# Optimization experiments

Hardware: AMD Instinct MI355X
Metric: run time of the kernel (lower is better)

The kernel has to match this reference:

```python
import jax, jax.numpy as jnp
import numpy as np

B, S, D = 8, 4096, 256
NUM_WINDOW = 8
WIN = S // NUM_WINDOW          # 512
H = 2                          # num_heads
K = D                          # key_dim = d_model per source
DFF = 1024
LN_EPS = 1e-3                  # keras LayerNormalization default epsilon


def _layer_norm(x, g, b):
    mu = jnp.mean(x, axis=-1, keepdims=True)
    var = jnp.mean(jnp.square(x - mu), axis=-1, keepdims=True)
    return (x - mu) * jax.lax.rsqrt(var + LN_EPS) * g + b


def setup_inputs() -> dict:
    key = jax.random.key(0)
    ks = jax.random.split(key, 12)
    s = 0.02
    inp = {
        "x": jax.random.normal(ks[0], (B, S, D), dtype=jnp.float32),
        # MHA projections (keras MultiHeadAttention layout)
        "Wq": jax.random.normal(ks[1], (D, H, K), dtype=jnp.float32) * s,
        "bq": jnp.zeros((H, K), dtype=jnp.float32),
        "Wk": jax.random.normal(ks[2], (D, H, K), dtype=jnp.float32) * s,
        "bk": jnp.zeros((H, K), dtype=jnp.float32),
        "Wv": jax.random.normal(ks[3], (D, H, K), dtype=jnp.float32) * s,
        "bv": jnp.zeros((H, K), dtype=jnp.float32),
        "Wo": jax.random.normal(ks[4], (H, K, D), dtype=jnp.float32) * s,
        "bo": jnp.zeros((D,), dtype=jnp.float32),
        "ln1_g": jnp.ones((D,), dtype=jnp.float32),
        "ln1_b": jnp.zeros((D,), dtype=jnp.float32),
        # FeedForward
        "W1": jax.random.normal(ks[5], (D, DFF), dtype=jnp.float32) * s,
        "b1": jnp.zeros((DFF,), dtype=jnp.float32),
        "W2": jax.random.normal(ks[6], (DFF, D), dtype=jnp.float32) * s,
        "b2": jnp.zeros((D,), dtype=jnp.float32),
        "ln2_g": jnp.ones((D,), dtype=jnp.float32),
        "ln2_b": jnp.zeros((D,), dtype=jnp.float32),
    }
    return inp


def reference(x, Wq, bq, Wk, bk, Wv, bv, Wo, bo, ln1_g, ln1_b,
              W1, b1, W2, b2, ln2_g, ln2_b):
    # --- Localized self-attention: block-diagonal over NUM_WINDOW windows ---
    xw = x.reshape(B, NUM_WINDOW, WIN, D)               # [b, w, s, d]
    q = jnp.einsum('bwsd,dhk->bwshk', xw, Wq) + bq      # [b, w, s, h, k]
    k = jnp.einsum('bwsd,dhk->bwshk', xw, Wk) + bk
    v = jnp.einsum('bwsd,dhk->bwshk', xw, Wv) + bv
    scores = jnp.einsum('bwshk,bwthk->bwhst', q, k) / jnp.sqrt(
        jnp.asarray(K, dtype=x.dtype))                  # [b, w, h, s, t]
    attn = jax.nn.softmax(scores, axis=-1)
    ctx = jnp.einsum('bwhst,bwthk->bwshk', attn, v)     # [b, w, s, h, k]
    attn_out = jnp.einsum('bwshk,hkd->bwsd', ctx, Wo) + bo
    attn_out = attn_out.reshape(B, S, D)                # concat over windows
    x = _layer_norm(x + attn_out, ln1_g, ln1_b)
    # --- FeedForward (dropout inactive at inference) ---
    h = jax.nn.relu(x @ W1 + b1)
    ff = h @ W2 + b2
    return _layer_norm(x + ff, ln2_g, ln2_b)
```

## Files before the change

kernel.cpp:

```cpp
#include <hip/hip_runtime.h>

typedef unsigned short u16;
typedef short short8 __attribute__((ext_vector_type(8)));
typedef float f32x4 __attribute__((ext_vector_type(4)));

#define AS1C const __attribute__((address_space(1))) void*
#define AS3P __attribute__((address_space(3))) void*
#define VMW(n) asm volatile("s_waitcnt vmcnt(" #n ")" ::: "memory")
#define SCHEDB() __builtin_amdgcn_sched_barrier(0)

__device__ __forceinline__ u16 f2b(float f) {
  unsigned u = __float_as_uint(f);
  return (u16)((u + 0x7fffu + ((u >> 16) & 1u)) >> 16);
}
__device__ __forceinline__ float b2f(u16 h) {
  return __uint_as_float((unsigned)h << 16);
}

#define BB 8
#define SS 4096
#define DD 256
#define MTOK (BB*SS)

#define OFF_WQKVT  ((size_t)0)
#define OFF_WOT    ((size_t)786432)
#define OFF_W1T    ((size_t)1048576)
#define OFF_W2T    ((size_t)1572864)
#define OFF_BQKV   ((size_t)2097152)
#define OFF_XB     ((size_t)2103296)
#define OFF_QKV    ((size_t)18880512)
#define OFF_YB     ((size_t)52434944)
#define OFF_HB     ((size_t)69212160)
#define OFF_VT     ((size_t)119543808)
#define OFF_CTX    ((size_t)153098240)

__global__ __launch_bounds__(256) void cast_x_kernel(const float* __restrict__ x,
                                                     u16* __restrict__ xb) {
  size_t i = ((size_t)blockIdx.x * 256 + threadIdx.x) * 4;
  float4 v = *(const float4*)(x + i);
  ushort4 o;
  o.x = f2b(v.x); o.y = f2b(v.y); o.z = f2b(v.z); o.w = f2b(v.w);
  *(ushort4*)(xb + i) = o;
}

__global__ __launch_bounds__(256) void prep_w_kernel(
    const float* __restrict__ Wq, const float* __restrict__ Wk, const float* __restrict__ Wv,
    const float* __restrict__ Wo, const float* __restrict__ W1, const float* __restrict__ W2,
    const float* __restrict__ bq, const float* __restrict__ bk, const float* __restrict__ bv,
    u16* __restrict__ wqkvt, u16* __restrict__ wot, u16* __restrict__ w1t,
    u16* __restrict__ w2t, float* __restrict__ bqkv)
{
  for (int i = blockIdx.x * 256 + threadIdx.x; i < 1050112; i += 1024 * 256) {
    if (i < 393216) {
      int n = i >> 8, d = i & 255;
      const float* W = (n < 512) ? Wq : (n < 1024) ? Wk : Wv;
      int nn = n & 511;
      wqkvt[i] = f2b(W[d * 512 + nn]);
    } else if (i < 524288) {
      int j = i - 393216;
      int dout = j >> 9, hk = j & 511;
      wot[j] = f2b(Wo[hk * 256 + dout]);
    } else if (i < 786432) {
      int j = i - 524288;
      int f = j >> 8, d = j & 255;
      w1t[j] = f2b(W1[d * 1024 + f]);
    } else if (i < 1048576) {
      int j = i - 786432;
      int d = j >> 10, f = j & 1023;
      w2t[j] = f2b(W2[f * 256 + d]);
    } else {
      int n = i - 1048576;
      bqkv[n] = (n < 512) ? bq[n] : (n < 1024) ? bk[n - 512] : bv[n - 1024];
    }
  }
}

__global__ __launch_bounds__(256) void gemm_nres(
    const u16* __restrict__ A, const u16* __restrict__ BT,
    const float* __restrict__ bias, u16* __restrict__ C,
    u16* __restrict__ vt, int N, int vbase, int relu)
{
  __shared__ __align__(16) u16 lds[24576];
  const int tid = threadIdx.x, lane = tid & 63, wid = tid >> 6;
  const int ln = lane & 15, quad = lane >> 4;
  const int pn = blockIdx.x >> 5;
  const int mg = blockIdx.x & 31;
  const int wno = (wid >> 1) << 5;
  const int wmo = (wid & 1) << 4;
  const long mbase = (long)mg << 10;
  const int nb = pn << 6;
  const u16* Bp = BT + (size_t)nb * 256;
  const u16* Ap = A + (size_t)mbase * 256;

#pragma unroll
  for (int p = 0; p < 8; p++) {
    const int s = p * 256 + tid;
    const int row = s >> 5, pc = s & 31;
    const int c = pc ^ (row & 31);
    __builtin_amdgcn_global_load_lds(
        (AS1C)(Bp + (size_t)row * 256 + c * 8), (AS3P)(lds + s * 8), 16, 0, 0);
  }
  __syncthreads();
  short8 breg[2][8];
#pragma unroll
  for (int j = 0; j < 2; j++) {
    const int row = wno + j * 16 + ln;
#pragma unroll
    for (int ks = 0; ks < 8; ks++)
      breg[j][ks] = *(const short8*)(lds + row * 256 + (((ks << 2) + quad) ^ (row & 31)) * 8);
  }
  const float4 b40 = *(const float4*)(bias + nb + wno + quad * 4);
  const float4 b41 = *(const float4*)(bias + nb + wno + 16 + quad * 4);
  __syncthreads();

#pragma unroll
  for (int sl = 0; sl < 2; sl++) {
    const u16* As = Ap + (size_t)sl * 32 * 256;
#pragma unroll
    for (int p = 0; p < 4; p++) {
      const int s = p * 256 + tid;
      const int row = s >> 5, pc = s & 31;
      const int c = pc ^ (row & 31);
      __builtin_amdgcn_global_load_lds(
          (AS1C)(As + (size_t)row * 256 + c * 8), (AS3P)(lds + sl * 8192 + s * 8), 16, 0, 0);
    }
  }

  for (int it = 0; it < 32; it++) {
    if (it == 0)            VMW(4);
    else if (it == 31)      VMW(0);
    else if (nb < vbase)    VMW(6);
    else                    VMW(12);
    SCHEDB();
    __builtin_amdgcn_s_barrier();
    SCHEDB();
    const u16* Ab = lds + (it % 3) * 8192;
    f32x4 acc[2];
    acc[0] = (f32x4){0.f, 0.f, 0.f, 0.f};
    acc[1] = (f32x4){0.f, 0.f, 0.f, 0.f};
    const int r0 = wmo + ln;
#pragma unroll
    for (int ks = 0; ks < 8; ks++) {
      const short8 a0 = *(const short8*)(Ab + r0 * 256 + (((ks << 2) + quad) ^ (r0 & 31)) * 8);
      acc[0] = __builtin_amdgcn_mfma_f32_16x16x32_bf16(breg[0][ks], a0, acc[0], 0, 0, 0);
      acc[1] = __builtin_amdgcn_mfma_f32_16x16x32_bf16(breg[1][ks], a0, acc[1], 0, 0, 0);
    }
    const long m = mbase + it * 32 + wmo + ln;
    if (nb < vbase) {
#pragma unroll
      for (int j = 0; j < 2; j++) {
        const int n0 = nb + wno + j * 16 + quad * 4;
        f32x4 v = acc[j];
        const float4 b4 = j ? b41 : b40;
        v[0] += b4.x; v[1] += b4.y; v[2] += b4.z; v[3] += b4.w;
        if (relu) {
#pragma unroll
          for (int r = 0; r < 4; r++) v[r] = fmaxf(v[r], 0.f);
        }
        ushort4 ob;
        ob.x = f2b(v[0]); ob.y = f2b(v[1]); ob.z = f2b(v[2]); ob.w = f2b(v[3]);
        *(ushort4*)(C + (size_t)m * N + n0) = ob;
      }
    } else {
      const int bw = (int)(m >> 9), t = (int)(m & 511);
#pragma unroll
      for (int j = 0; j < 2; j++) {
        const int n0 = nb + wno + j * 16 + quad * 4;
        const int rel = n0 - vbase;
        const int h = rel >> 8, k0 = rel & 255;
        u16* vp = vt + (size_t)(bw * 2 + h) * 131072 + (size_t)k0 * 512 + t;
        const float4 b4 = j ? b41 : b40;
        vp[0]    = f2b(acc[j][0] + b4.x);
        vp[512]  = f2b(acc[j][1] + b4.y);
        vp[1024] = f2b(acc[j][2] + b4.z);
        vp[1536] = f2b(acc[j][3] + b4.w);
      }
    }
    if (it < 30) {
      const u16* An = Ap + (size_t)(it + 2) * 32 * 256;
      u16* Ax = lds + ((it + 2) % 3) * 8192;
#pragma unroll
      for (int p = 0; p < 4; p++) {
        const int s = p * 256 + tid;
        const int row = s >> 5, pc = s & 31;
        const int c = pc ^ (row & 31);
        __builtin_amdgcn_global_load_lds(
            (AS1C)(An + (size_t)row * 256 + c * 8), (AS3P)(Ax + s * 8), 16, 0, 0);
      }
    }
  }
}

__global__ __launch_bounds__(512, 4) void attn_fused(const u16* __restrict__ qkv,
                                                     const u16* __restrict__ vt,
                                                     u16* __restrict__ ctx)
{
  __shared__ __align__(16) u16 lds[38912];
  const int tid = threadIdx.x, lane = tid & 63, wid = tid >> 6;
  const int ln = lane & 15, quad = lane >> 4;
  const int bat = blockIdx.x & 127, mt = blockIdx.x >> 7;
  const int bw = bat >> 1, h = bat & 1;
  const u16* Qb = qkv + (size_t)bw * 786432 + (size_t)h * 256 + (size_t)(mt * 64) * 1536;
  const u16* Kb = qkv + (size_t)bw * 786432 + 512 + (size_t)h * 256;
  const u16* Vb = vt + (size_t)bat * 131072;
  const int wn = wid * 64;
  const int qsw = (ln >> 1) & 3;
  float* red1 = (float*)(lds + 36864);
  float* red2 = red1 + 512;

  f32x4 acc[4][4];
#pragma unroll
  for (int i = 0; i < 4; i++)
#pragma unroll
    for (int j = 0; j < 4; j++) acc[i][j] = (f32x4){0.f, 0.f, 0.f, 0.f};

  if (tid < 256) {
    const int row = tid >> 2;
    const int c = (tid & 3) ^ ((row >> 1) & 3);
    __builtin_amdgcn_global_load_lds(
        (AS1C)(Qb + (size_t)row * 1536 + c * 8), (AS3P)(lds + tid * 8), 16, 0, 0);
  }
#pragma unroll
  for (int p = 0; p < 4; p++) {
    const int s = p * 512 + tid;
    const int row = s >> 2;
    const int c = (s & 3) ^ ((row >> 1) & 3);
    __builtin_amdgcn_global_load_lds(
        (AS1C)(Kb + (size_t)row * 1536 + c * 8), (AS3P)(lds + 4096 + s * 8), 16, 0, 0);
  }

  for (int ki = 0; ki < 8; ki++) {
    const int cur = ki & 1;
    __syncthreads();
    if (ki < 7) {
      const int kt = (ki + 1) * 32, nxt = cur ^ 1;
      if (tid < 256) {
        const int row = tid >> 2;
        const int c = (tid & 3) ^ ((row >> 1) & 3);
        __builtin_amdgcn_global_load_lds(
            (AS1C)(Qb + (size_t)row * 1536 + kt + c * 8),
            (AS3P)(lds + nxt * 2048 + tid * 8), 16, 0, 0);
      }
#pragma unroll
      for (int p = 0; p < 4; p++) {
        const int s = p * 512 + tid;
        const int row = s >> 2;
        const int c = (s & 3) ^ ((row >> 1) & 3);
        __builtin_amdgcn_global_load_lds(
            (AS1C)(Kb + (size_t)row * 1536 + kt + c * 8),
            (AS3P)(lds + 4096 + nxt * 16384 + s * 8), 16, 0, 0);
      }
    }
    short8 a[4], b[4];
#pragma unroll
    for (int i = 0; i < 4; i++)
      a[i] = *(const short8*)(lds + cur * 2048 + ((i * 16 + ln) * 4 + (quad ^ qsw)) * 8);
#pragma unroll
    for (int j = 0; j < 4; j++)
      b[j] = *(const short8*)(lds + 4096 + cur * 16384 + ((wn + j * 16 + ln) * 4 + (quad ^ qsw)) * 8);
    __builtin_amdgcn_s_setprio(1);
#pragma unroll
    for (int i = 0; i < 4; i++)
#pragma unroll
      for (int j = 0; j < 4; j++)
        acc[i][j] = __builtin_amdgcn_mfma_f32_16x16x32_bf16(b[j], a[i], acc[i][j], 0, 0, 0);
    __builtin_amdgcn_s_setprio(0);
  }

  float rowmax[4], rowsum[4];
#pragma unroll
  for (int i = 0; i < 4; i++) {
    float m = -1e30f;
#pragma unroll
    for (int j = 0; j < 4; j++)
#pragma unroll
      for (int r = 0; r < 4; r++) m = fmaxf(m, acc[i][j][r]);
    m = fmaxf(m, __shfl_xor(m, 16));
    m = fmaxf(m, __shfl_xor(m, 32));
    if (quad == 0) red1[wid * 64 + i * 16 + ln] = m;
  }
  __syncthreads();

#pragma unroll
  for (int p = 0; p < 4; p++) {
    const int s = p * 512 + tid;
    const int row = s >> 3, pc = s & 7;
    const int cc = pc ^ (row & 7);
    __builtin_amdgcn_global_load_lds(
        (AS1C)(Vb + (size_t)row * 512 + cc * 8), (AS3P)(lds + s * 8), 16, 0, 0);
  }

#pragma unroll
  for (int i = 0; i < 4; i++) {
    float m = -1e30f;
#pragma unroll
    for (int w = 0; w < 8; w++) m = fmaxf(m, red1[w * 64 + i * 16 + ln]);
    rowmax[i] = m;
  }
#pragma unroll
  for (int i = 0; i < 4; i++) {
    float s = 0.f;
#pragma unroll
    for (int j = 0; j < 4; j++)
#pragma unroll
      for (int r = 0; r < 4; r++) {
        const float e = __expf((acc[i][j][r] - rowmax[i]) * 0.0625f);
        acc[i][j][r] = e; s += e;
      }
    s += __shfl_xor(s, 16);
    s += __shfl_xor(s, 32);
    if (quad == 0) red2[wid * 64 + i * 16 + ln] = s;
  }
  __syncthreads();
#pragma unroll
  for (int i = 0; i < 4; i++) {
    float s = 0.f;
#pragma unroll
    for (int w = 0; w < 8; w++) s += red2[w * 64 + i * 16 + ln];
    rowsum[i] = 1.f / s;
  }

  ushort4 pb[4][4];
#pragma unroll
  for (int i = 0; i < 4; i++)
#pragma unroll
    for (int j = 0; j < 4; j++) {
      pb[i][j].x = f2b(acc[i][j][0] * rowsum[i]);
      pb[i][j].y = f2b(acc[i][j][1] * rowsum[i]);
      pb[i][j].z = f2b(acc[i][j][2] * rowsum[i]);
      pb[i][j].w = f2b(acc[i][j][3] * rowsum[i]);
    }

  u16* Pb = lds + 32768;
  const int wno = wid * 32;
  f32x4 o[4][2];
#pragma unroll
  for (int i = 0; i < 4; i++) {
    o[i][0] = (f32x4){0.f, 0.f, 0.f, 0.f};
    o[i][1] = (f32x4){0.f, 0.f, 0.f, 0.f};
  }

  for (int c = 0; c < 8; c++) {
    __syncthreads();
    if (wid == c) {
#pragma unroll
      for (int i = 0; i < 4; i++)
#pragma unroll
        for (int j = 0; j < 4; j++)
          *(ushort4*)(Pb + (i * 16 + ln) * 72 + j * 16 + quad * 4) = pb[i][j];
    }
    __syncthreads();
    if (c < 7) {
      const int nb = (c + 1) & 1;
#pragma unroll
      for (int p = 0; p < 4; p++) {
        const int s = p * 512 + tid;
        const int row = s >> 3, pc = s & 7;
        const int cc = pc ^ (row & 7);
        __builtin_amdgcn_global_load_lds(
            (AS1C)(Vb + (size_t)row * 512 + (c + 1) * 64 + cc * 8),
            (AS3P)(lds + nb * 16384 + s * 8), 16, 0, 0);
      }
    }
    const u16* Vc = lds + (c & 1) * 16384;
    __builtin_amdgcn_s_setprio(1);
#pragma unroll
    for (int ks = 0; ks < 2; ks++) {
      short8 ap[4];
#pragma unroll
      for (int i = 0; i < 4; i++)
        ap[i] = *(const short8*)(Pb + (i * 16 + ln) * 72 + ks * 32 + quad * 8);
#pragma unroll
      for (int j = 0; j < 2; j++) {
        const int kV = wno + j * 16 + ln;
        const short8 bv = *(const short8*)(Vc + kV * 64 + (((ks << 2) + quad) ^ (kV & 7)) * 8);
#pragma unroll
        for (int i = 0; i < 4; i++)
          o[i][j] = __builtin_amdgcn_mfma_f32_16x16x32_bf16(bv, ap[i], o[i][j], 0, 0, 0);
      }
    }
    __builtin_amdgcn_s_setprio(0);
  }

  const size_t tokr0 = (size_t)bw * 512 + mt * 64;
#pragma unroll
  for (int i = 0; i < 4; i++) {
    const size_t row = tokr0 + i * 16 + ln;
#pragma unroll
    for (int j = 0; j < 2; j++) {
      const int col = h * 256 + wno + j * 16 + quad * 4;
      ushort4 ob;
      ob.x = f2b(o[i][j][0]); ob.y = f2b(o[i][j][1]);
      ob.z = f2b(o[i][j][2]); ob.w = f2b(o[i][j][3]);
      *(ushort4*)(ctx + row * 512 + col) = ob;
    }
  }
}

__global__ __launch_bounds__(256) void gemm_ln(
    const u16* __restrict__ A, const u16* __restrict__ BT,
    const float* __restrict__ bias, const u16* __restrict__ residb,
    const float* __restrict__ g, const float* __restrict__ beta,
    float* __restrict__ yout, u16* __restrict__ ybout, int K)
{
  __shared__ __align__(16) u16 ring[3][10240];
  __shared__ float redS[4][64], redQ[4][64];
  const int tid = threadIdx.x, lane = tid & 63, wid = tid >> 6;
  const int ln = lane & 15, quad = lane >> 4;
  const int qsw = (ln >> 1) & 3;
  const long bm = (long)blockIdx.x * 64;
  const int wn = wid * 64;
  const u16* Ab = A + (size_t)bm * K;
  const int nk = K >> 5;

  f32x4 acc[4][4];
#pragma unroll
  for (int i = 0; i < 4; i++)
#pragma unroll
    for (int j = 0; j < 4; j++) acc[i][j] = (f32x4){0.f, 0.f, 0.f, 0.f};

#pragma unroll
  for (int sl = 0; sl < 2; sl++) {
    const int kt = sl * 32;
    const int row = tid >> 2;
    const int c = (tid & 3) ^ ((row >> 1) & 3);
    __builtin_amdgcn_global_load_lds(
        (AS1C)(Ab + (size_t)row * K + kt + c * 8), (AS3P)(&ring[sl][0] + tid * 8), 16, 0, 0);
#pragma unroll
    for (int p = 0; p < 4; p++) {
      const int s = p * 256 + tid;
      const int br = s >> 2;
      const int bc = (s & 3) ^ ((br >> 1) & 3);
      __builtin_amdgcn_global_load_lds(
          (AS1C)(BT + (size_t)br * K + kt + bc * 8), (AS3P)(&ring[sl][2048] + s * 8), 16, 0, 0);
    }
  }

  for (int kti = 0; kti < nk; kti++) {
    if (kti + 1 < nk) VMW(5); else VMW(0);
    SCHEDB();
    __builtin_amdgcn_s_barrier();
    SCHEDB();
    const u16* Rc = &ring[kti % 3][0];
    short8 a[4], b[4];
#pragma unroll
    for (int i = 0; i < 4; i++)
      a[i] = *(const short8*)(Rc + ((i * 16 + ln) * 4 + (quad ^ qsw)) * 8);
#pragma unroll
    for (int j = 0; j < 4; j++)
      b[j] = *(const short8*)(Rc + 2048 + ((wn + j * 16 + ln) * 4 + (quad ^ qsw)) * 8);
    __builtin_amdgcn_s_setprio(1);
#pragma unroll
    for (int i = 0; i < 4; i++)
#pragma unroll
      for (int j = 0; j < 4; j++)
        acc[i][j] = __builtin_amdgcn_mfma_f32_16x16x32_bf16(b[j], a[i], acc[i][j], 0, 0, 0);
    __builtin_amdgcn_s_setprio(0);
    if (kti + 2 < nk) {
      const int kt = (kti + 2) * 32;
      u16* Rn = &ring[(kti + 2) % 3][0];
      const int row = tid >> 2;
      const int c = (tid & 3) ^ ((row >> 1) & 3);
      __builtin_amdgcn_global_load_lds(
          (AS1C)(Ab + (size_t)row * K + kt + c * 8), (AS3P)(Rn + tid * 8), 16, 0, 0);
#pragma unroll
      for (int p = 0; p < 4; p++) {
        const int s = p * 256 + tid;
        const int br = s >> 2;
        const int bc = (s & 3) ^ ((br >> 1) & 3);
        __builtin_amdgcn_global_load_lds(
            (AS1C)(BT + (size_t)br * K + kt + bc * 8), (AS3P)(Rn + 2048 + s * 8), 16, 0, 0);
      }
    }
  }

#pragma unroll
  for (int i = 0; i < 4; i++) {
    const long gm = bm + i * 16 + ln;
    float s = 0.f, q = 0.f;
#pragma unroll
    for (int j = 0; j < 4; j++) {
      const int n0 = wn + j * 16 + quad * 4;
      const float4 b4 = *(const float4*)(bias + n0);
      const ushort4 r4 = *(const ushort4*)(residb + (size_t)gm * 256 + n0);
      acc[i][j][0] += b4.x + b2f(r4.x);
      acc[i][j][1] += b4.y + b2f(r4.y);
      acc[i][j][2] += b4.z + b2f(r4.z);
      acc[i][j][3] += b4.w + b2f(r4.w);
#pragma unroll
      for (int r = 0; r < 4; r++) { s += acc[i][j][r]; q += acc[i][j][r] * acc[i][j][r]; }
    }
    s += __shfl_xor(s, 16); s += __shfl_xor(s, 32);
    q += __shfl_xor(q, 16); q += __shfl_xor(q, 32);
    if (quad == 0) { redS[wid][i * 16 + ln] = s; redQ[wid][i * 16 + ln] = q; }
  }
  __syncthreads();
#pragma unroll
  for (int i = 0; i < 4; i++) {
    const long gm = bm + i * 16 + ln;
    float s = 0.f, q = 0.f;
#pragma unroll
    for (int w = 0; w < 4; w++) { s += redS[w][i * 16 + ln]; q += redQ[w][i * 16 + ln]; }
    const float mu = s * (1.f / 256.f);
    const float inv = rsqrtf(q * (1.f / 256.f) - mu * mu + 1e-3f);
#pragma unroll
    for (int j = 0; j < 4; j++) {
      const int n0 = wn + j * 16 + quad * 4;
      const float4 gg = *(const float4*)(g + n0);
      const float4 bb = *(const float4*)(beta + n0);
      float o0 = (acc[i][j][0] - mu) * inv * gg.x + bb.x;
      float o1 = (acc[i][j][1] - mu) * inv * gg.y + bb.y;
      float o2 = (acc[i][j][2] - mu) * inv * gg.z + bb.z;
      float o3 = (acc[i][j][3] - mu) * inv * gg.w + bb.w;
      const size_t off = (size_t)gm * 256 + n0;
      if (yout) {
        float4 o4; o4.x = o0; o4.y = o1; o4.z = o2; o4.w = o3;
        *(float4*)(yout + off) = o4;
      }
      if (ybout) {
        ushort4 ob;
        ob.x = f2b(o0); ob.y = f2b(o1); ob.z = f2b(o2); ob.w = f2b(o3);
        *(ushort4*)(ybout + off) = ob;
      }
    }
  }
}

extern "C" void kernel_launch(void* const* d_in, const int* in_sizes, int n_in,
                              void* d_out, int out_size, void* d_ws, size_t ws_size,
                              hipStream_t stream) {
  (void)in_sizes; (void)n_in; (void)out_size; (void)ws_size;
  const float* x    = (const float*)d_in[0];
  const float* Wq   = (const float*)d_in[1];
  const float* bq   = (const float*)d_in[2];
  const float* Wk   = (const float*)d_in[3];
  const float* bk   = (const float*)d_in[4];
  const float* Wv   = (const float*)d_in[5];
  const float* bv   = (const float*)d_in[6];
  const float* Wo   = (const float*)d_in[7];
  const float* bo   = (const float*)d_in[8];
  const float* ln1g = (const float*)d_in[9];
  const float* ln1b = (const float*)d_in[10];
  const float* W1   = (const float*)d_in[11];
  const float* b1   = (const float*)d_in[12];
  const float* W2   = (const float*)d_in[13];
  const float* b2   = (const float*)d_in[14];
  const float* ln2g = (const float*)d_in[15];
  const float* ln2b = (const float*)d_in[16];
  float* out = (float*)d_out;

  char* ws = (char*)d_ws;
  u16*   WQKVT = (u16*)(ws + OFF_WQKVT);
  u16*   WOT   = (u16*)(ws + OFF_WOT);
  u16*   W1T   = (u16*)(ws + OFF_W1T);
  u16*   W2T   = (u16*)(ws + OFF_W2T);
  float* BQKV  = (float*)(ws + OFF_BQKV);
  u16*   XB    = (u16*)(ws + OFF_XB);
  u16*   QKV   = (u16*)(ws + OFF_QKV);
  u16*   YB    = (u16*)(ws + OFF_YB);
  u16*   HB    = (u16*)(ws + OFF_HB);
  u16*   VT    = (u16*)(ws + OFF_VT);
  u16*   CTX   = (u16*)(ws + OFF_CTX);

  cast_x_kernel<<<8192, 256, 0, stream>>>(x, XB);
  prep_w_kernel<<<1024, 256, 0, stream>>>(Wq, Wk, Wv, Wo, W1, W2, bq, bk, bv,
                                          WQKVT, WOT, W1T, W2T, BQKV);
  gemm_nres<<<768, 256, 0, stream>>>(XB, WQKVT, BQKV, QKV, VT, 1536, 1024, 0);
  attn_fused<<<1024, 512, 0, stream>>>(QKV, VT, CTX);
  gemm_ln<<<512, 256, 0, stream>>>(CTX, WOT, bo, XB, ln1g, ln1b, nullptr, YB, 512);
  gemm_nres<<<512, 256, 0, stream>>>(YB, W1T, b1, HB, nullptr, 1024, 1 << 30, 1);
  gemm_ln<<<512, 256, 0, stream>>>(HB, W2T, b2, YB, ln2g, ln2b, out, nullptr, 1024);
}
```

Before: 319.3 us.

## Tile weight prep via LDS transpose and widen GEMM N-tile to 128

The weight-prep kernel now transposes and casts weights in 64x64 tiles through shared memory, so reads and writes are coalesced, replacing the strided gather with 1024 blocks. The QKV/FFN1 GEMM widens each block's N tile from 64 to 128 and halves its M span, so each A tile in LDS feeds twice as many MFMAs. It also raises wave priority around the MFMA loop. The trade-off is more registers for B fragments and accumulators, which may reduce occupancy, and changed waitcnt thresholds that must match the new load counts.

```diff
diff --git a/kernel.cpp b/kernel.cpp
--- a/kernel.cpp
+++ b/kernel.cpp
@@ -50,28 +50,32 @@
     u16* __restrict__ wqkvt, u16* __restrict__ wot, u16* __restrict__ w1t,
     u16* __restrict__ w2t, float* __restrict__ bqkv)
 {
-  for (int i = blockIdx.x * 256 + threadIdx.x; i < 1050112; i += 1024 * 256) {
-    if (i < 393216) {
-      int n = i >> 8, d = i & 255;
-      const float* W = (n < 512) ? Wq : (n < 1024) ? Wk : Wv;
-      int nn = n & 511;
-      wqkvt[i] = f2b(W[d * 512 + nn]);
-    } else if (i < 524288) {
-      int j = i - 393216;
-      int dout = j >> 9, hk = j & 511;
-      wot[j] = f2b(Wo[hk * 256 + dout]);
-    } else if (i < 786432) {
-      int j = i - 524288;
-      int f = j >> 8, d = j & 255;
-      w1t[j] = f2b(W1[d * 1024 + f]);
-    } else if (i < 1048576) {
-      int j = i - 786432;
-      int d = j >> 10, f = j & 1023;
-      w2t[j] = f2b(W2[f * 256 + d]);
-    } else {
-      int n = i - 1048576;
+  __shared__ float t[64 * 65];
+  const int tid = threadIdx.x;
+  const int b = blockIdx.x;
+  if (b == 256) {
+    for (int n = tid; n < 1536; n += 256)
       bqkv[n] = (n < 512) ? bq[n] : (n < 1024) ? bk[n - 512] : bv[n - 1024];
-    }
+    return;
+  }
+  const float* src; u16* dst; int R, C, tb;
+  if (b < 96)       { const int m = b / 32; src = (m == 0) ? Wq : (m == 1) ? Wk : Wv;
+                      dst = wqkvt + m * 512 * 256; R = 256; C = 512; tb = b & 31; }
+  else if (b < 128) { src = Wo; dst = wot;  R = 512;  C = 256;  tb = b - 96; }
+  else if (b < 192) { src = W1; dst = w1t;  R = 256;  C = 1024; tb = b - 128; }
+  else              { src = W2; dst = w2t;  R = 1024; C = 256;  tb = b - 192; }
+  const int tc = C >> 6;
+  const int tr = tb / tc, tcc = tb % tc;
+#pragma unroll
+  for (int p = 0; p < 16; p++) {
+    const int idx = p * 256 + tid, r = idx >> 6, c = idx & 63;
+    t[r * 65 + c] = src[(size_t)(tr * 64 + r) * C + tcc * 64 + c];
+  }
+  __syncthreads();
+#pragma unroll
+  for (int p = 0; p < 16; p++) {
+    const int idx = p * 256 + tid, c = idx >> 6, r = idx & 63;
+    dst[(size_t)(tcc * 64 + c) * R + tr * 64 + r] = f2b(t[r * 65 + c]);
   }
 }
 
@@ -80,20 +84,20 @@
     const float* __restrict__ bias, u16* __restrict__ C,
     u16* __restrict__ vt, int N, int vbase, int relu)
 {
-  __shared__ __align__(16) u16 lds[24576];
+  __shared__ __align__(16) u16 lds[32768];
   const int tid = threadIdx.x, lane = tid & 63, wid = tid >> 6;
   const int ln = lane & 15, quad = lane >> 4;
-  const int pn = blockIdx.x >> 5;
-  const int mg = blockIdx.x & 31;
-  const int wno = (wid >> 1) << 5;
+  const int pn = blockIdx.x >> 6;
+  const int mg = blockIdx.x & 63;
+  const int wno = (wid >> 1) << 6;
   const int wmo = (wid & 1) << 4;
-  const long mbase = (long)mg << 10;
-  const int nb = pn << 6;
+  const long mbase = (long)mg << 9;
+  const int nb = pn << 7;
   const u16* Bp = BT + (size_t)nb * 256;
   const u16* Ap = A + (size_t)mbase * 256;
 
 #pragma unroll
-  for (int p = 0; p < 8; p++) {
+  for (int p = 0; p < 16; p++) {
     const int s = p * 256 + tid;
     const int row = s >> 5, pc = s & 31;
     const int c = pc ^ (row & 31);
@@ -101,16 +105,18 @@
         (AS1C)(Bp + (size_t)row * 256 + c * 8), (AS3P)(lds + s * 8), 16, 0, 0);
   }
   __syncthreads();
-  short8 breg[2][8];
-#pragma unroll
-  for (int j = 0; j < 2; j++) {
+  short8 breg[4][8];
+#pragma unroll
+  for (int j = 0; j < 4; j++) {
     const int row = wno + j * 16 + ln;
 #pragma unroll
     for (int ks = 0; ks < 8; ks++)
       breg[j][ks] = *(const short8*)(lds + row * 256 + (((ks << 2) + quad) ^ (row & 31)) * 8);
   }
-  const float4 b40 = *(const float4*)(bias + nb + wno + quad * 4);
-  const float4 b41 = *(const float4*)(bias + nb + wno + 16 + quad * 4);
+  float4 b4h[4];
+#pragma unroll
+  for (int j = 0; j < 4; j++)
+    b4h[j] = *(const float4*)(bias + nb + wno + j * 16 + quad * 4);
   __syncthreads();
 
 #pragma unroll
@@ -126,32 +132,35 @@
     }
   }
 
-  for (int it = 0; it < 32; it++) {
+  for (int it = 0; it < 16; it++) {
     if (it == 0)            VMW(4);
-    else if (it == 31)      VMW(0);
-    else if (nb < vbase)    VMW(6);
-    else                    VMW(12);
+    else if (it == 15)      VMW(0);
+    else if (nb < vbase)    VMW(8);
+    else                    VMW(20);
     SCHEDB();
     __builtin_amdgcn_s_barrier();
     SCHEDB();
     const u16* Ab = lds + (it % 3) * 8192;
-    f32x4 acc[2];
-    acc[0] = (f32x4){0.f, 0.f, 0.f, 0.f};
-    acc[1] = (f32x4){0.f, 0.f, 0.f, 0.f};
+    f32x4 acc[4];
+#pragma unroll
+    for (int j = 0; j < 4; j++) acc[j] = (f32x4){0.f, 0.f, 0.f, 0.f};
     const int r0 = wmo + ln;
+    __builtin_amdgcn_s_setprio(1);
 #pragma unroll
     for (int ks = 0; ks < 8; ks++) {
       const short8 a0 = *(const short8*)(Ab + r0 * 256 + (((ks << 2) + quad) ^ (r0 & 31)) * 8);
-      acc[0] = __builtin_amdgcn_mfma_f32_16x16x32_bf16(breg[0][ks], a0, acc[0], 0, 0, 0);
-      acc[1] = __builtin_amdgcn_mfma_f32_16x16x32_bf16(breg[1][ks], a0, acc[1], 0, 0, 0);
-    }
+#pragma unroll
+      for (int j = 0; j < 4; j++)
+        acc[j] = __builtin_amdgcn_mfma_f32_16x16x32_bf16(breg[j][ks], a0, acc[j], 0, 0, 0);
+    }
+    __builtin_amdgcn_s_setprio(0);
     const long m = mbase + it * 32 + wmo + ln;
     if (nb < vbase) {
 #pragma unroll
-      for (int j = 0; j < 2; j++) {
+      for (int j = 0; j < 4; j++) {
         const int n0 = nb + wno + j * 16 + quad * 4;
         f32x4 v = acc[j];
-        const float4 b4 = j ? b41 : b40;
+        const float4 b4 = b4h[j];
         v[0] += b4.x; v[1] += b4.y; v[2] += b4.z; v[3] += b4.w;
         if (relu) {
 #pragma unroll
@@ -164,19 +173,19 @@
     } else {
       const int bw = (int)(m >> 9), t = (int)(m & 511);
 #pragma unroll
-      for (int j = 0; j < 2; j++) {
+      for (int j = 0; j < 4; j++) {
         const int n0 = nb + wno + j * 16 + quad * 4;
         const int rel = n0 - vbase;
         const int h = rel >> 8, k0 = rel & 255;
         u16* vp = vt + (size_t)(bw * 2 + h) * 131072 + (size_t)k0 * 512 + t;
-        const float4 b4 = j ? b41 : b40;
+        const float4 b4 = b4h[j];
         vp[0]    = f2b(acc[j][0] + b4.x);
         vp[512]  = f2b(acc[j][1] + b4.y);
         vp[1024] = f2b(acc[j][2] + b4.z);
         vp[1536] = f2b(acc[j][3] + b4.w);
       }
     }
-    if (it < 30) {
+    if (it < 14) {
       const u16* An = Ap + (size_t)(it + 2) * 32 * 256;
       u16* Ax = lds + ((it + 2) % 3) * 8192;
 #pragma unroll
@@ -563,8 +572,8 @@
   u16*   CTX   = (u16*)(ws + OFF_CTX);
 
   cast_x_kernel<<<8192, 256, 0, stream>>>(x, XB);
-  prep_w_kernel<<<1024, 256, 0, stream>>>(Wq, Wk, Wv, Wo, W1, W2, bq, bk, bv,
-                                          WQKVT, WOT, W1T, W2T, BQKV);
+  prep_w_kernel<<<257, 256, 0, stream>>>(Wq, Wk, Wv, Wo, W1, W2, bq, bk, bv,
+                                         WQKVT, WOT, W1T, W2T, BQKV);
   gemm_nres<<<768, 256, 0, stream>>>(XB, WQKVT, BQKV, QKV, VT, 1536, 1024, 0);
   attn_fused<<<1024, 512, 0, stream>>>(QKV, VT, CTX);
   gemm_ln<<<512, 256, 0, stream>>>(CTX, WOT, bo, XB, ln1g, ln1b, nullptr, YB, 512);
```

New measurement: 306.9 us, median of 2. 3.9% less time.
